# Kernel optimization log

Hardware: AMD Instinct MI355X
Metric: run time of the kernel (lower is better)

## Reference

```python
import jax, jax.numpy as jnp
import numpy as np


def cross_scan(x):
    # x: (B, D, H, W) -> xs: (B, 8, D, L)  (row, col, rev-row, rev-col, diag, antidiag, rev-diag, rev-antidiag)
    B, D, H, W = x.shape
    L = H * W
    hs = jnp.arange(H)[:, None]
    ws = jnp.arange(W)[None, :]
    x0 = x.reshape(B, D, L)                          # row-major
    x1 = jnp.swapaxes(x, 2, 3).reshape(B, D, L)      # column-major
    gd = x[:, :, hs, (hs + ws) % W]                  # diagonal gather (B,D,H,W)
    ga = x[:, :, hs, (ws - hs) % W]                  # antidiagonal gather
    x4 = jnp.swapaxes(gd, -1, -2).reshape(B, D, L)
    x5 = jnp.swapaxes(ga, -1, -2).reshape(B, D, L)
    return jnp.stack([x0, x1, x0[..., ::-1], x1[..., ::-1],
                      x4, x5, x4[..., ::-1], x5[..., ::-1]], axis=1)


def cross_merge(ys, H, W):
    # ys: (B, 8, D, L) -> (B, D, L), inverse-scatter + sum of all 8 directions
    B, K, D, L = ys.shape
    hs = jnp.arange(H)[:, None]
    ws = jnp.arange(W)[None, :]
    y = ys[:, 0] + ys[:, 2, :, ::-1]
    yt = (ys[:, 1] + ys[:, 3, :, ::-1]).reshape(B, D, W, H)
    y = y + jnp.swapaxes(yt, -1, -2).reshape(B, D, L)
    # diagonal scatter: result[h, w'] = t[h, (w'-h) % W]
    td = jnp.swapaxes((ys[:, 4] + ys[:, 6, :, ::-1]).reshape(B, D, W, H), -1, -2)
    y = y + td[:, :, hs, (ws - hs) % W].reshape(B, D, L)
    # antidiagonal scatter: result[h, w'] = t[h, (w'+h) % W]
    ta = jnp.swapaxes((ys[:, 5] + ys[:, 7, :, ::-1]).reshape(B, D, W, H), -1, -2)
    y = y + ta[:, :, hs, (ws + hs) % W].reshape(B, D, L)
    return y


def selective_scan(u, delta, A, Bs, Cs, Ds):
    # u, delta: (B, KD, L); A: (KD, N); Bs, Cs: (B, K, N, L); Ds: (KD,)
    Bb, KD, L = u.shape
    K = Bs.shape[1]
    Dh = KD // K
    N = A.shape[1]
    u_ = jnp.moveaxis(u.reshape(Bb, K, Dh, L), -1, 0)        # (L,B,K,Dh)
    d_ = jnp.moveaxis(delta.reshape(Bb, K, Dh, L), -1, 0)
    B_ = jnp.moveaxis(Bs, -1, 0)                              # (L,B,K,N)
    C_ = jnp.moveaxis(Cs, -1, 0)
    A_ = A.reshape(K, Dh, N)

    def step(h, inp):
        u_t, d_t, b_t, c_t = inp
        dA = jnp.exp(d_t[..., None] * A_)                     # (B,K,Dh,N)
        h = h * dA + (d_t * u_t)[..., None] * b_t[:, :, None, :]
        y = jnp.einsum('bkdn,bkn->bkd', h, c_t)
        return h, y

    h0 = jnp.zeros((Bb, K, Dh, N), u.dtype)
    _, ys = jax.lax.scan(step, h0, (u_, d_, B_, C_))          # ys: (L,B,K,Dh)
    ys = jnp.moveaxis(ys, 0, -1).reshape(Bb, KD, L)
    return ys + u * Ds[None, :, None]


def setup_inputs() -> dict:
    key = jax.random.key(0)
    ks = jax.random.split(key, 6)
    B, D, H, W = 2, 192, 64, 64
    K, N, R = 8, 16, 6
    x = jax.random.normal(ks[0], (B, D, H, W), jnp.float32)
    x_proj_weight = jax.random.normal(ks[1], (K, R + 2 * N, D), jnp.float32) * (1.0 / np.sqrt(D))
    dt_projs_weight = jax.random.normal(ks[2], (K, D, R), jnp.float32) * (0.1 / np.sqrt(R))
    dt_projs_bias = jax.random.normal(ks[3], (K, D), jnp.float32) * 0.1
    A_logs = jax.random.uniform(ks[4], (K * D, N), jnp.float32)
    Ds = jax.random.normal(ks[5], (K * D,), jnp.float32)
    ln_w = jnp.ones((D,), jnp.float32)
    ln_b = jnp.zeros((D,), jnp.float32)
    return {"x": x, "x_proj_weight": x_proj_weight, "dt_projs_weight": dt_projs_weight,
            "dt_projs_bias": dt_projs_bias, "A_logs": A_logs, "Ds": Ds,
            "ln_w": ln_w, "ln_b": ln_b}


def reference(x, x_proj_weight, dt_projs_weight, dt_projs_bias, A_logs, Ds, ln_w, ln_b):
    B, D, H, W = x.shape
    K = x_proj_weight.shape[0]
    N = A_logs.shape[1]
    R = dt_projs_weight.shape[2]
    L = H * W
    xs = cross_scan(x)                                            # (B,K,D,L)
    x_dbl = jnp.einsum('bkdl,kcd->bkcl', xs, x_proj_weight)       # (B,K,R+2N,L)
    dts, Bs, Cs = jnp.split(x_dbl, [R, R + N], axis=2)
    dts = jnp.einsum('bkrl,kdr->bkdl', dts, dt_projs_weight)      # (B,K,D,L)
    u = xs.reshape(B, K * D, L)
    delta = jax.nn.softplus(dts.reshape(B, K * D, L) + dt_projs_bias.reshape(1, K * D, 1))
    A = -jnp.exp(A_logs)                                          # (KD,N)
    ys = selective_scan(u, delta, A, Bs, Cs, Ds)                  # (B,KD,L)
    y = cross_merge(ys.reshape(B, K, D, L), H, W)                 # (B,D,L)
    y = jnp.swapaxes(y, 1, 2)                                     # (B,L,D)
    mu = y.mean(-1, keepdims=True)
    var = y.var(-1, keepdims=True)
    y = (y - mu) / jnp.sqrt(var + 1e-5) * ln_w + ln_b             # out_norm (LayerNorm)
    return y.reshape(B, H, W, D)
```

## Files before the change

kernel.cpp:

```cpp
#include <hip/hip_runtime.h>
#include <math.h>

#define BB   2
#define DD   192
#define LL   4096
#define KK   8
#define NN   16
#define RR   6
#define C38  38
#define CPAD 40
#define NCH  64
#define CLEN (LL / NCH)
#define NCHAN (BB * KK * DD)

__device__ __forceinline__ float fexp2(float x) { return __builtin_amdgcn_exp2f(x); }
__device__ __forceinline__ float flog2(float x) { return __builtin_amdgcn_logf(x); }

__device__ __forceinline__ float softplus_f(float x) {
  return fmaxf(x, 0.f) + 0.69314718f * flog2(1.f + fexp2(-1.44269504f * fabsf(x)));
}

__device__ __forceinline__ int src_index(int k, int l) {
  int ll = (k & 2) ? (LL - 1 - l) : l;
  int kb = k & 5;
  if (kb == 0) return ll;
  int h = ll & 63, w = ll >> 6;
  if (kb == 1) return (h << 6) + w;
  if (kb == 4) return (h << 6) + ((h + w) & 63);
  return (h << 6) + ((w - h) & 63);
}

__global__ __launch_bounds__(256) void transpose_x(const float* __restrict__ x,
                                                   float* __restrict__ xT,
                                                   float* __restrict__ Y) {
  __shared__ float tile[32][33];
  int b  = blockIdx.z;
  int p0 = blockIdx.x * 32;
  int d0 = blockIdx.y * 32;
  int tx = threadIdx.x, ty = threadIdx.y;
  #pragma unroll
  for (int i = 0; i < 32; i += 8)
    tile[ty + i][tx] = x[((size_t)(b * DD + d0 + ty + i)) * LL + p0 + tx];
  __syncthreads();
  #pragma unroll
  for (int i = 0; i < 32; i += 8) {
    size_t idx = ((size_t)(b * LL + p0 + ty + i)) * DD + d0 + tx;
    xT[idx] = tile[tx][ty + i];
    Y[idx]  = 0.f;
  }
}

__global__ __launch_bounds__(256) void proj_kernel(const float* __restrict__ xT,
                                                   const float* __restrict__ W,
                                                   float* __restrict__ xdbl) {
  int k = blockIdx.y, b = blockIdx.z;
  int tx = threadIdx.x;
  int slot = tx & 127, chalf = tx >> 7;
  int l_a = blockIdx.x * 256 + slot;
  int l_b = l_a + 128;
  __shared__ __align__(16) float sm[DD * CPAD];
  for (int i = tx; i < C38 * DD; i += 256) {
    int c = i / DD, dq = i - c * DD;
    sm[dq * CPAD + c] = W[(k * C38 + c) * DD + dq];
  }
  for (int dq = tx; dq < DD; dq += 256) { sm[dq * CPAD + 38] = 0.f; sm[dq * CPAD + 39] = 0.f; }
  __syncthreads();

  int p_a = src_index(k, l_a);
  int p_b = src_index(k, l_b);
  const float4* xa4 = (const float4*)(xT + ((size_t)b * LL + p_a) * DD);
  const float4* xb4 = (const float4*)(xT + ((size_t)b * LL + p_b) * DD);
  const float* wbase = sm + chalf * 20;
  float4 accA[5], accB[5];
  #pragma unroll
  for (int c = 0; c < 5; ++c) {
    accA[c] = make_float4(0.f, 0.f, 0.f, 0.f);
    accB[c] = make_float4(0.f, 0.f, 0.f, 0.f);
  }

  for (int d4 = 0; d4 < 48; ++d4) {
    float4 xa = xa4[d4];
    float4 xb = xb4[d4];
    #pragma unroll
    for (int s = 0; s < 4; ++s) {
      float xsa = (s == 0) ? xa.x : (s == 1) ? xa.y : (s == 2) ? xa.z : xa.w;
      float xsb = (s == 0) ? xb.x : (s == 1) ? xb.y : (s == 2) ? xb.z : xb.w;
      const float4* w4 = (const float4*)(wbase + (d4 * 4 + s) * CPAD);
      #pragma unroll
      for (int c = 0; c < 5; ++c) {
        float4 wv = w4[c];
        accA[c].x = fmaf(wv.x, xsa, accA[c].x);
        accA[c].y = fmaf(wv.y, xsa, accA[c].y);
        accA[c].z = fmaf(wv.z, xsa, accA[c].z);
        accA[c].w = fmaf(wv.w, xsa, accA[c].w);
        accB[c].x = fmaf(wv.x, xsb, accB[c].x);
        accB[c].y = fmaf(wv.y, xsb, accB[c].y);
        accB[c].z = fmaf(wv.z, xsb, accB[c].z);
        accB[c].w = fmaf(wv.w, xsb, accB[c].w);
      }
    }
  }

  float4* oA = (float4*)(xdbl + ((size_t)((b * KK + k) * LL) + l_a) * CPAD + chalf * 20);
  float4* oB = (float4*)(xdbl + ((size_t)((b * KK + k) * LL) + l_b) * CPAD + chalf * 20);
  #pragma unroll
  for (int c = 0; c < 5; ++c) { oA[c] = accA[c]; oB[c] = accB[c]; }
}

template <bool FINAL>
__global__ __launch_bounds__(384, 4) void scan_kernel(
    const float* __restrict__ xT, const float* __restrict__ xdbl,
    const float* __restrict__ A_logs, const float* __restrict__ dtw,
    const float* __restrict__ dtb, const float* __restrict__ Ds,
    float* __restrict__ Sarr, float* __restrict__ Qarr, float* __restrict__ Y) {
  constexpr int ROWF  = FINAL ? 40 : 24;
  constexpr int ROWF2 = ROWF / 2;
  constexpr int SRCF2 = FINAL ? 19 : 11;

  __shared__ __align__(16) float rows[CLEN * ROWF];

  const int lane  = threadIdx.x;
  const int ng    = lane >> 5;
  const int dd    = threadIdx.y;
  const int tid   = dd * 64 + lane;
  const int bk    = blockIdx.x;
  const int chunk = blockIdx.y;
  const int b = bk >> 3, k = bk & 7;
  const int d  = dd * 32 + (lane & 31);
  const int kd = k * DD + d;
  const int ch = bk * DD + d;
  const int l0 = chunk * CLEN;

  {
    const float2* src2 = (const float2*)(xdbl + ((size_t)(bk * LL) + l0) * CPAD);
    float2* dst2 = (float2*)rows;
    for (int i = tid; i < CLEN * SRCF2; i += 384) {
      int r = i / SRCF2, c = i - r * SRCF2;
      dst2[r * ROWF2 + c + (c >= 3)] = src2[r * (CPAD / 2) + c];
    }
  }

  float An2[8];
  {
    const float* ap = A_logs + (size_t)kd * NN + ng * 8;
    #pragma unroll
    for (int j = 0; j < 8; ++j) An2[j] = -__expf(ap[j]) * 1.44269504f;
  }
  float wdt[RR];
  #pragma unroll
  for (int r = 0; r < RR; ++r) wdt[r] = dtw[kd * RR + r];
  const float bias = dtb[kd];
  const float dval = FINAL ? Ds[kd] : 0.f;

  float h[8];
  if constexpr (FINAL) {
    const float* h0p = Qarr + ((size_t)chunk * NCHAN + ch) * NN + ng * 8;
    #pragma unroll
    for (int j = 0; j < 8; ++j) h[j] = h0p[j];
  } else {
    #pragma unroll
    for (int j = 0; j < 8; ++j) h[j] = 0.f;
  }

  const float* xTb = xT + (size_t)b * LL * DD + d;
  float S = 0.f;

  __syncthreads();

  auto STEP = [&](int t, int p, float u) {
    const float* row = rows + t * ROWF;
    float dts = bias;
    dts = fmaf(row[0], wdt[0], dts);
    dts = fmaf(row[1], wdt[1], dts);
    dts = fmaf(row[2], wdt[2], dts);
    dts = fmaf(row[3], wdt[3], dts);
    dts = fmaf(row[4], wdt[4], dts);
    dts = fmaf(row[5], wdt[5], dts);
    float spv = softplus_f(dts);
    float du = spv * u;
    const float4* bq = (const float4*)(row + 8 + ng * 8);
    float4 b0 = bq[0], b1 = bq[1];
    float Bvv[8] = {b0.x, b0.y, b0.z, b0.w, b1.x, b1.y, b1.z, b1.w};
    #pragma unroll
    for (int j = 0; j < 8; ++j) {
      float e = fexp2(spv * An2[j]);
      h[j] = fmaf(h[j], e, du * Bvv[j]);
    }
    if constexpr (FINAL) {
      const float4* cq = (const float4*)(row + 24 + ng * 8);
      float4 c0 = cq[0], c1 = cq[1];
      float Cvv[8] = {c0.x, c0.y, c0.z, c0.w, c1.x, c1.y, c1.z, c1.w};
      float y = 0.f;
      #pragma unroll
      for (int j = 0; j < 8; ++j) y = fmaf(h[j], Cvv[j], y);
      y += __shfl_xor(y, 32, 64);
      if (ng == 0) {
        atomicAdd(&Y[(size_t)(b * LL + p) * DD + d], fmaf(u, dval, y));
      }
    } else {
      S += spv;
    }
  };

  int ppA[4], ppB[4];
  float uuA[4], uuB[4];
  #pragma unroll
  for (int s = 0; s < 4; ++s) {
    int p = src_index(k, l0 + s);
    ppA[s] = p; uuA[s] = xTb[(size_t)p * DD];
  }
  for (int tb = 0; tb < CLEN; tb += 8) {
    #pragma unroll
    for (int s = 0; s < 4; ++s) {
      int p = src_index(k, l0 + tb + 4 + s);
      ppB[s] = p; uuB[s] = xTb[(size_t)p * DD];
    }
    #pragma unroll
    for (int s = 0; s < 4; ++s) STEP(tb + s, ppA[s], uuA[s]);
    int nb = (tb + 8 < CLEN) ? tb + 8 : 0;
    #pragma unroll
    for (int s = 0; s < 4; ++s) {
      int p = src_index(k, l0 + nb + s);
      ppA[s] = p; uuA[s] = xTb[(size_t)p * DD];
    }
    #pragma unroll
    for (int s = 0; s < 4; ++s) STEP(tb + 4 + s, ppB[s], uuB[s]);
  }

  if constexpr (!FINAL) {
    if (ng == 0) Sarr[(size_t)chunk * NCHAN + ch] = S;
    float* qp = Qarr + ((size_t)chunk * NCHAN + ch) * NN + ng * 8;
    #pragma unroll
    for (int j = 0; j < 8; ++j) qp[j] = h[j];
  }
}

__global__ __launch_bounds__(256) void stitch_kernel(const float* __restrict__ Sarr,
                                                     float* __restrict__ Qarr,
                                                     const float* __restrict__ A_logs) {
  const int t  = blockIdx.x * 256 + threadIdx.x;
  const int ch = t >> 4, n = t & 15;
  const int kd = ch % (KK * DD);
  const float An2 = -__expf(A_logs[(size_t)kd * NN + n]) * 1.44269504f;

  float q[8], Sv[8];
  #pragma unroll
  for (int i = 0; i < 8; ++i) {
    q[i]  = Qarr[(size_t)i * (NCHAN * NN) + t];
    Sv[i] = Sarr[(size_t)i * NCHAN + ch];
  }
  float h = 0.f;
  for (int cb = 0; cb < NCH; cb += 8) {
    #pragma unroll
    for (int i = 0; i < 8; ++i) {
      const int c = cb + i;
      Qarr[(size_t)c * (NCHAN * NN) + t] = h;
      h = fmaf(fexp2(An2 * Sv[i]), h, q[i]);
      const int cn = c + 8;
      if (cn < NCH) {
        q[i]  = Qarr[(size_t)cn * (NCHAN * NN) + t];
        Sv[i] = Sarr[(size_t)cn * NCHAN + ch];
      }
    }
  }
}

__global__ __launch_bounds__(256) void ln_kernel(const float* __restrict__ Y,
                                                 const float* __restrict__ lw,
                                                 const float* __restrict__ lb,
                                                 float* __restrict__ out) {
  int lane = threadIdx.x & 63;
  int row = blockIdx.x * 4 + (threadIdx.x >> 6);
  const float* yr = Y + (size_t)row * DD;
  float v0 = yr[lane], v1 = yr[lane + 64], v2 = yr[lane + 128];
  float s1 = v0 + v1 + v2;
  float s2 = v0 * v0 + v1 * v1 + v2 * v2;
  #pragma unroll
  for (int m = 32; m >= 1; m >>= 1) {
    s1 += __shfl_xor(s1, m, 64);
    s2 += __shfl_xor(s2, m, 64);
  }
  float mu = s1 * (1.f / DD);
  float var = s2 * (1.f / DD) - mu * mu;
  float inv = rsqrtf(var + 1e-5f);
  float* orow = out + (size_t)row * DD;
  orow[lane]       = (v0 - mu) * inv * lw[lane]       + lb[lane];
  orow[lane + 64]  = (v1 - mu) * inv * lw[lane + 64]  + lb[lane + 64];
  orow[lane + 128] = (v2 - mu) * inv * lw[lane + 128] + lb[lane + 128];
}

extern "C" void kernel_launch(void* const* d_in, const int* in_sizes, int n_in,
                              void* d_out, int out_size, void* d_ws, size_t ws_size,
                              hipStream_t stream) {
  const float* x      = (const float*)d_in[0];
  const float* xpw    = (const float*)d_in[1];
  const float* dtw    = (const float*)d_in[2];
  const float* dtb    = (const float*)d_in[3];
  const float* A_logs = (const float*)d_in[4];
  const float* Ds     = (const float*)d_in[5];
  const float* ln_w   = (const float*)d_in[6];
  const float* ln_b   = (const float*)d_in[7];
  float* out = (float*)d_out;

  float* ws   = (float*)d_ws;
  float* xT   = ws;
  float* xdbl = xT + 1572864;
  float* Y    = xdbl + 2621440;
  float* Sarr = Y + 1572864;
  float* Qarr = Sarr + 196608;

  transpose_x<<<dim3(LL / 32, DD / 32, BB), dim3(32, 8), 0, stream>>>(x, xT, Y);
  proj_kernel<<<dim3(LL / 256, KK, BB), 256, 0, stream>>>(xT, xpw, xdbl);
  scan_kernel<false><<<dim3(BB * KK, NCH), dim3(64, 6), 0, stream>>>(
      xT, xdbl, A_logs, dtw, dtb, Ds, Sarr, Qarr, Y);
  stitch_kernel<<<(NCHAN * NN) / 256, 256, 0, stream>>>(Sarr, Qarr, A_logs);
  scan_kernel<true><<<dim3(BB * KK, NCH), dim3(64, 6), 0, stream>>>(
      xT, xdbl, A_logs, dtw, dtb, Ds, Sarr, Qarr, Y);
  ln_kernel<<<(BB * LL) / 4, 256, 0, stream>>>(Y, ln_w, ln_b, out);
}
```

Before: 223.0 us.

## Stage per-chunk u values and source indices in shared memory for scan kernel

Each scan block now bulk-loads all u values for its chunk (CLEN x DD floats) and the permuted source indices into LDS before the recurrence. This replaces the per-step register prefetch of scattered global loads with coalesced cooperative loads. The dt row reads become vector loads and the C dot-product uses split accumulators. The extra shared memory (64*192*4 bytes, about 48KB) cuts occupancy, and launch bounds drop from 4 to 2 blocks per CU to match.

```diff
diff --git a/kernel.cpp b/kernel.cpp
--- a/kernel.cpp
+++ b/kernel.cpp
@@ -108,7 +108,7 @@
 }
 
 template <bool FINAL>
-__global__ __launch_bounds__(384, 4) void scan_kernel(
+__global__ __launch_bounds__(384, 2) void scan_kernel(
     const float* __restrict__ xT, const float* __restrict__ xdbl,
     const float* __restrict__ A_logs, const float* __restrict__ dtw,
     const float* __restrict__ dtb, const float* __restrict__ Ds,
@@ -118,6 +118,8 @@
   constexpr int SRCF2 = FINAL ? 19 : 11;
 
   __shared__ __align__(16) float rows[CLEN * ROWF];
+  __shared__ __align__(16) float uu_s[CLEN * DD];
+  __shared__ int p_s[CLEN];
 
   const int lane  = threadIdx.x;
   const int ng    = lane >> 5;
@@ -131,6 +133,7 @@
   const int ch = bk * DD + d;
   const int l0 = chunk * CLEN;
 
+  if (tid < CLEN) p_s[tid] = src_index(k, l0 + tid);
   {
     const float2* src2 = (const float2*)(xdbl + ((size_t)(bk * LL) + l0) * CPAD);
     float2* dst2 = (float2*)rows;
@@ -152,6 +155,16 @@
   const float bias = dtb[kd];
   const float dval = FINAL ? Ds[kd] : 0.f;
 
+  __syncthreads();
+
+  {
+    const float* xTbase = xT + (size_t)b * LL * DD;
+    for (int i = tid; i < CLEN * DD; i += 384) {
+      int t = i / DD, dq = i - t * DD;
+      uu_s[i] = xTbase[(size_t)p_s[t] * DD + dq];
+    }
+  }
+
   float h[8];
   if constexpr (FINAL) {
     const float* h0p = Qarr + ((size_t)chunk * NCHAN + ch) * NN + ng * 8;
@@ -161,70 +174,56 @@
     #pragma unroll
     for (int j = 0; j < 8; ++j) h[j] = 0.f;
   }
-
-  const float* xTb = xT + (size_t)b * LL * DD + d;
   float S = 0.f;
 
   __syncthreads();
 
-  auto STEP = [&](int t, int p, float u) {
+  auto STEP = [&](int t) {
     const float* row = rows + t * ROWF;
+    float4 dt4 = *(const float4*)(row);
+    float2 dt2 = *(const float2*)(row + 4);
     float dts = bias;
-    dts = fmaf(row[0], wdt[0], dts);
-    dts = fmaf(row[1], wdt[1], dts);
-    dts = fmaf(row[2], wdt[2], dts);
-    dts = fmaf(row[3], wdt[3], dts);
-    dts = fmaf(row[4], wdt[4], dts);
-    dts = fmaf(row[5], wdt[5], dts);
+    dts = fmaf(dt4.x, wdt[0], dts);
+    dts = fmaf(dt4.y, wdt[1], dts);
+    dts = fmaf(dt4.z, wdt[2], dts);
+    dts = fmaf(dt4.w, wdt[3], dts);
+    dts = fmaf(dt2.x, wdt[4], dts);
+    dts = fmaf(dt2.y, wdt[5], dts);
     float spv = softplus_f(dts);
+    float u = uu_s[t * DD + d];
     float du = spv * u;
     const float4* bq = (const float4*)(row + 8 + ng * 8);
     float4 b0 = bq[0], b1 = bq[1];
-    float Bvv[8] = {b0.x, b0.y, b0.z, b0.w, b1.x, b1.y, b1.z, b1.w};
-    #pragma unroll
-    for (int j = 0; j < 8; ++j) {
-      float e = fexp2(spv * An2[j]);
-      h[j] = fmaf(h[j], e, du * Bvv[j]);
-    }
+    h[0] = fmaf(h[0], fexp2(spv * An2[0]), du * b0.x);
+    h[1] = fmaf(h[1], fexp2(spv * An2[1]), du * b0.y);
+    h[2] = fmaf(h[2], fexp2(spv * An2[2]), du * b0.z);
+    h[3] = fmaf(h[3], fexp2(spv * An2[3]), du * b0.w);
+    h[4] = fmaf(h[4], fexp2(spv * An2[4]), du * b1.x);
+    h[5] = fmaf(h[5], fexp2(spv * An2[5]), du * b1.y);
+    h[6] = fmaf(h[6], fexp2(spv * An2[6]), du * b1.z);
+    h[7] = fmaf(h[7], fexp2(spv * An2[7]), du * b1.w);
     if constexpr (FINAL) {
       const float4* cq = (const float4*)(row + 24 + ng * 8);
       float4 c0 = cq[0], c1 = cq[1];
-      float Cvv[8] = {c0.x, c0.y, c0.z, c0.w, c1.x, c1.y, c1.z, c1.w};
-      float y = 0.f;
-      #pragma unroll
-      for (int j = 0; j < 8; ++j) y = fmaf(h[j], Cvv[j], y);
+      float y0 = h[0] * c0.x, y1 = h[1] * c0.y;
+      float y2 = h[2] * c0.z, y3 = h[3] * c0.w;
+      y0 = fmaf(h[4], c1.x, y0);
+      y1 = fmaf(h[5], c1.y, y1);
+      y2 = fmaf(h[6], c1.z, y2);
+      y3 = fmaf(h[7], c1.w, y3);
+      float y = (y0 + y1) + (y2 + y3);
       y += __shfl_xor(y, 32, 64);
       if (ng == 0) {
-        atomicAdd(&Y[(size_t)(b * LL + p) * DD + d], fmaf(u, dval, y));
+        atomicAdd(&Y[(size_t)(b * LL + p_s[t]) * DD + d], fmaf(u, dval, y));
       }
     } else {
       S += spv;
     }
   };
 
-  int ppA[4], ppB[4];
-  float uuA[4], uuB[4];
-  #pragma unroll
-  for (int s = 0; s < 4; ++s) {
-    int p = src_index(k, l0 + s);
-    ppA[s] = p; uuA[s] = xTb[(size_t)p * DD];
-  }
   for (int tb = 0; tb < CLEN; tb += 8) {
     #pragma unroll
-    for (int s = 0; s < 4; ++s) {
-      int p = src_index(k, l0 + tb + 4 + s);
-      ppB[s] = p; uuB[s] = xTb[(size_t)p * DD];
-    }
-    #pragma unroll
-    for (int s = 0; s < 4; ++s) STEP(tb + s, ppA[s], uuA[s]);
-    int nb = (tb + 8 < CLEN) ? tb + 8 : 0;
-    #pragma unroll
-    for (int s = 0; s < 4; ++s) {
-      int p = src_index(k, l0 + nb + s);
-      ppA[s] = p; uuA[s] = xTb[(size_t)p * DD];
-    }
-    #pragma unroll
-    for (int s = 0; s < 4; ++s) STEP(tb + 4 + s, ppB[s], uuB[s]);
+    for (int s = 0; s < 8; ++s) STEP(tb + s);
   }
 
   if constexpr (!FINAL) {
```

Result: slower. 269.0 us (+20.6%).

## Fold chunk-state stitch into final scan pass, dropping separate stitch kernel

Applied to the files above, without the earlier changes.

Removes the stitch kernel that sequentially combined per-chunk end states into chunk initial states. Each block of the final scan pass now recomputes its own initial state by folding over all preceding chunks' decay sums and states. This saves one kernel launch and the Qarr rewrite round trip. The cost is redundant, quadratic-in-chunk-count work and reads in the final pass, where late chunks iterate up to 63 times before scanning.

```diff
diff --git a/kernel.cpp b/kernel.cpp
--- a/kernel.cpp
+++ b/kernel.cpp
@@ -153,13 +153,22 @@
   const float dval = FINAL ? Ds[kd] : 0.f;
 
   float h[8];
+  #pragma unroll
+  for (int j = 0; j < 8; ++j) h[j] = 0.f;
   if constexpr (FINAL) {
-    const float* h0p = Qarr + ((size_t)chunk * NCHAN + ch) * NN + ng * 8;
-    #pragma unroll
-    for (int j = 0; j < 8; ++j) h[j] = h0p[j];
-  } else {
-    #pragma unroll
-    for (int j = 0; j < 8; ++j) h[j] = 0.f;
+    for (int j = 0; j < chunk; ++j) {
+      float Sj = Sarr[(size_t)j * NCHAN + ch];
+      const float4* qp = (const float4*)(Qarr + ((size_t)j * NCHAN + ch) * NN + ng * 8);
+      float4 q0 = qp[0], q1 = qp[1];
+      h[0] = fmaf(fexp2(An2[0] * Sj), h[0], q0.x);
+      h[1] = fmaf(fexp2(An2[1] * Sj), h[1], q0.y);
+      h[2] = fmaf(fexp2(An2[2] * Sj), h[2], q0.z);
+      h[3] = fmaf(fexp2(An2[3] * Sj), h[3], q0.w);
+      h[4] = fmaf(fexp2(An2[4] * Sj), h[4], q1.x);
+      h[5] = fmaf(fexp2(An2[5] * Sj), h[5], q1.y);
+      h[6] = fmaf(fexp2(An2[6] * Sj), h[6], q1.z);
+      h[7] = fmaf(fexp2(An2[7] * Sj), h[7], q1.w);
+    }
   }
 
   const float* xTb = xT + (size_t)b * LL * DD + d;
@@ -235,36 +244,6 @@
   }
 }
 
-__global__ __launch_bounds__(256) void stitch_kernel(const float* __restrict__ Sarr,
-                                                     float* __restrict__ Qarr,
-                                                     const float* __restrict__ A_logs) {
-  const int t  = blockIdx.x * 256 + threadIdx.x;
-  const int ch = t >> 4, n = t & 15;
-  const int kd = ch % (KK * DD);
-  const float An2 = -__expf(A_logs[(size_t)kd * NN + n]) * 1.44269504f;
-
-  float q[8], Sv[8];
-  #pragma unroll
-  for (int i = 0; i < 8; ++i) {
-    q[i]  = Qarr[(size_t)i * (NCHAN * NN) + t];
-    Sv[i] = Sarr[(size_t)i * NCHAN + ch];
-  }
-  float h = 0.f;
-  for (int cb = 0; cb < NCH; cb += 8) {
-    #pragma unroll
-    for (int i = 0; i < 8; ++i) {
-      const int c = cb + i;
-      Qarr[(size_t)c * (NCHAN * NN) + t] = h;
-      h = fmaf(fexp2(An2 * Sv[i]), h, q[i]);
-      const int cn = c + 8;
-      if (cn < NCH) {
-        q[i]  = Qarr[(size_t)cn * (NCHAN * NN) + t];
-        Sv[i] = Sarr[(size_t)cn * NCHAN + ch];
-      }
-    }
-  }
-}
-
 __global__ __launch_bounds__(256) void ln_kernel(const float* __restrict__ Y,
                                                  const float* __restrict__ lw,
                                                  const float* __restrict__ lb,
@@ -313,7 +292,6 @@
   proj_kernel<<<dim3(LL / 256, KK, BB), 256, 0, stream>>>(xT, xpw, xdbl);
   scan_kernel<false><<<dim3(BB * KK, NCH), dim3(64, 6), 0, stream>>>(
       xT, xdbl, A_logs, dtw, dtb, Ds, Sarr, Qarr, Y);
-  stitch_kernel<<<(NCHAN * NN) / 256, 256, 0, stream>>>(Sarr, Qarr, A_logs);
   scan_kernel<true><<<dim3(BB * KK, NCH), dim3(64, 6), 0, stream>>>(
       xT, xdbl, A_logs, dtw, dtb, Ds, Sarr, Qarr, Y);
   ln_kernel<<<(BB * LL) / 4, 256, 0, stream>>>(Y, ln_w, ln_b, out);
```

Result: slower. 237.6 us (+6.5%).
